# Optimization experiments

Measured on AMD Instinct MI355X. Metric: run time of the kernel, lower is better.

The kernel has to match this reference:

```python
import jax, jax.numpy as jnp
import numpy as np

B = 4          # clouds per batch
N_PER = 8192   # points per cloud
RATIO = 0.5
M = int(N_PER * RATIO)   # sampled centroids per cloud
R = 0.2        # radius
K = 64         # max_num_neighbors
C_IN = 64


def setup_inputs() -> dict:
    key = jax.random.key(0)
    k1, k2, k3, k4 = jax.random.split(key, 4)
    N = B * N_PER
    x = jax.random.normal(k1, (N, C_IN), dtype=jnp.float32)
    pos = jax.random.uniform(k2, (N, 3), dtype=jnp.float32)  # unit cube
    batch = jnp.repeat(jnp.arange(B, dtype=jnp.int32), N_PER)
    W1 = jax.random.normal(k3, (C_IN + 3, 64), dtype=jnp.float32) * (1.0 / np.sqrt(C_IN + 3))
    b1 = jnp.zeros((64,), dtype=jnp.float32)
    W2 = jax.random.normal(k4, (64, 128), dtype=jnp.float32) * (1.0 / np.sqrt(64))
    b2 = jnp.zeros((128,), dtype=jnp.float32)
    return {"x": x, "pos": pos, "batch": batch, "W1": W1, "b1": b1, "W2": W2, "b2": b2}


def _fps(posb):
    """Farthest point sampling, vectorized over clouds. posb: [B, n, 3] -> idx [B, M]."""
    d0 = jnp.sum((posb - posb[:, :1]) ** 2, axis=-1)  # dist^2 to seed point 0: [B, n]

    def step(dists, _):
        far = jnp.argmax(dists, axis=1)                              # [B]
        newp = jnp.take_along_axis(posb, far[:, None, None], axis=1)  # [B, 1, 3]
        d = jnp.sum((posb - newp) ** 2, axis=-1)                      # [B, n]
        return jnp.minimum(dists, d), far.astype(jnp.int32)

    _, rest = jax.lax.scan(step, d0, None, length=M - 1)  # rest: [M-1, B]
    return jnp.concatenate([jnp.zeros((B, 1), jnp.int32), rest.T], axis=1)  # [B, M]


def reference(x, pos, batch, W1, b1, W2, b2):
    posb = pos.reshape(B, N_PER, 3)
    xb = x.reshape(B, N_PER, C_IN)

    # --- fps ---
    idx = _fps(posb)                                         # [B, M]
    q = jnp.take_along_axis(posb, idx[:, :, None], axis=1)   # sampled centroids [B, M, 3]

    # --- radius query: K nearest neighbors within radius R (same cloud) ---
    d2 = jnp.sum((q[:, :, None, :] - posb[:, None, :, :]) ** 2, axis=-1)  # [B, M, n]
    neg = jnp.where(d2 <= R * R, -d2, -jnp.inf)
    vals, nbr = jax.lax.top_k(neg, K)                        # [B, M, K]
    valid = vals > -jnp.inf                                  # neighbor mask

    # --- PointNetConv: gather -> MLP -> masked max aggregation ---
    bidx = jnp.arange(B)[:, None, None]
    xj = xb[bidx, nbr]                                       # [B, M, K, C_IN]
    rel = posb[bidx, nbr] - q[:, :, None, :]                 # [B, M, K, 3]
    feat = jnp.concatenate([xj, rel], axis=-1)               # [B, M, K, C_IN+3]
    h = jax.nn.relu(feat @ W1 + b1)                          # [B, M, K, 64]
    h = jax.nn.relu(h @ W2 + b2)                             # [B, M, K, 128]
    h = jnp.where(valid[..., None], h, -jnp.inf)
    out = jnp.max(h, axis=2)                                 # [B, M, 128]; self-edge guarantees >=1 valid

    x_out = out.reshape(B * M, 128)
    pos_out = q.reshape(B * M, 3)
    batch_out = jnp.repeat(jnp.arange(B, dtype=batch.dtype), M)
    return x_out, pos_out, batch_out
```

## Files before the change

### kernel.cpp

```cpp
#include <hip/hip_runtime.h>
#include <stdint.h>

#define NPER 8192
#define NB 4
#define MPER 4096
#define MTOT (NB*MPER)
#define KNB 64
#define CIN 64
#define R2C 0.04f

#define POSOUT_OFF (MTOT*128)
#define BATCH_OFF  (MTOT*128 + MTOT*3)


#define FPS_T 1024
#define PTS 8
#define NCELL 512

#define OFF_XS 0
#define OFF_YS (OFF_XS + NPER*4)
#define OFF_ZS (OFF_YS + NPER*4)
#define OFF_OS (OFF_ZS + NPER*4)
#define OFF_WIN (OFF_OS + NPER*2)
#define OFF_HIST (OFF_WIN + MPER*2)
#define OFF_SCAN (OFF_HIST + NCELL*4)
#define OFF_SLOT (OFF_SCAN + NCELL*4)
#define OFF_SID0 (OFF_SLOT + 24)
#define FPS_LDS  (OFF_SID0 + 8)

__device__ inline unsigned morton3(unsigned ix, unsigned iy, unsigned iz) {
  unsigned m = 0;
#pragma unroll
  for (int b = 0; b < 3; ++b)
    m |= (((ix >> b) & 1u) << (3*b + 2)) | (((iy >> b) & 1u) << (3*b + 1)) |
         (((iz >> b) & 1u) << (3*b));
  return m;
}

template<int CTRL>
__device__ __forceinline__ unsigned dppmax(unsigned v) {
  unsigned t = (unsigned)__builtin_amdgcn_update_dpp(
      0, (int)v, CTRL, 0xf, 0xf, true);
  return v > t ? v : t;
}
__device__ __forceinline__ unsigned wave_max_u32(unsigned v) {
  v = dppmax<0x111>(v);
  v = dppmax<0x112>(v);
  v = dppmax<0x114>(v);
  v = dppmax<0x118>(v);
  v = dppmax<0x142>(v);
  v = dppmax<0x143>(v);
  return (unsigned)__builtin_amdgcn_readlane((int)v, 63);
}

__global__ __launch_bounds__(1024) void k_fps(const float* __restrict__ pos,
                                              float* __restrict__ dout)
{
  extern __shared__ char smem[];
  float* Xs = (float*)(smem + OFF_XS);
  float* Ys = (float*)(smem + OFF_YS);
  float* Zs = (float*)(smem + OFF_ZS);
  unsigned short* Os = (unsigned short*)(smem + OFF_OS);
  unsigned short* winb = (unsigned short*)(smem + OFF_WIN);
  unsigned* hist = (unsigned*)(smem + OFF_HIST);
  unsigned* scanb = (unsigned*)(smem + OFF_SCAN);
  unsigned long long* slot3 = (unsigned long long*)(smem + OFF_SLOT);
  unsigned* sid0p = (unsigned*)(smem + OFF_SID0);

  const int b = blockIdx.x;
  const int tid = threadIdx.x;
  const float* pb = pos + (size_t)b * NPER * 3;
  float* qo = dout + POSOUT_OFF + (size_t)b * MPER * 3;

  if (tid < NCELL) hist[tid] = 0u;
  if (tid == 0) { slot3[0] = 0ull; slot3[1] = 0ull; slot3[2] = 0ull; }
  __syncthreads();

  float sxv[PTS], syv[PTS], szv[PTS];
  unsigned cellv[PTS];
#pragma unroll
  for (int k = 0; k < PTS; ++k) {
    int i = k * FPS_T + tid;
    sxv[k] = pb[i*3+0]; syv[k] = pb[i*3+1]; szv[k] = pb[i*3+2];
    unsigned ix = min(7u, (unsigned)(int)(sxv[k] * 8.0f));
    unsigned iy = min(7u, (unsigned)(int)(syv[k] * 8.0f));
    unsigned iz = min(7u, (unsigned)(int)(szv[k] * 8.0f));
    cellv[k] = morton3(ix, iy, iz);
    atomicAdd(&hist[cellv[k]], 1u);
  }
  __syncthreads();
  if (tid < NCELL) scanb[tid] = hist[tid];
  __syncthreads();
  for (int s = 1; s < NCELL; s <<= 1) {
    unsigned v = 0u;
    if (tid >= s && tid < NCELL) v = scanb[tid - s];
    __syncthreads();
    if (tid >= s && tid < NCELL) scanb[tid] += v;
    __syncthreads();
  }
  if (tid < NCELL) hist[tid] = scanb[tid] - hist[tid];
  __syncthreads();
#pragma unroll
  for (int k = 0; k < PTS; ++k) {
    unsigned dst = atomicAdd(&hist[cellv[k]], 1u);
    int orig = k * FPS_T + tid;
    Xs[dst] = sxv[k]; Ys[dst] = syv[k]; Zs[dst] = szv[k];
    Os[dst] = (unsigned short)orig;
    if (orig == 0) *sid0p = dst;
  }
  __syncthreads();
  float X[PTS], Y[PTS], Z[PTS], D[PTS];
  unsigned RK[PTS];
  float bxlo = 3.402823466e+38f, bylo = bxlo, bzlo = bxlo;
  float bxhi = -bxlo, byhi = bxhi, bzhi = bxhi;
#pragma unroll
  for (int k = 0; k < PTS; ++k) {
    int s = tid * PTS + k;
    X[k] = Xs[s]; Y[k] = Ys[s]; Z[k] = Zs[s];
    unsigned orig = Os[s];
    RK[k] = ((unsigned)(NPER - 1 - orig) << 13) | (unsigned)s;
    D[k] = 3.402823466e+38f;
    bxlo = fminf(bxlo, X[k]); bxhi = fmaxf(bxhi, X[k]);
    bylo = fminf(bylo, Y[k]); byhi = fmaxf(byhi, Y[k]);
    bzlo = fminf(bzlo, Z[k]); bzhi = fmaxf(bzhi, Z[k]);
  }

  unsigned long long tkey = 0ull, wkey = 0ull;
  float lmax = 3.402823466e+38f;
  unsigned sidx = *sid0p;
  for (int m = 1; m < MPER; ++m) {
    const float cx = Xs[sidx], cy = Ys[sidx], cz = Zs[sidx];
    if (tid == 0) winb[m-1] = (unsigned short)sidx;
    if (tid == 1) slot3[(m+1) % 3] = 0ull;
    float ax = fmaxf(fmaxf(__fsub_rn(bxlo, cx), __fsub_rn(cx, bxhi)), 0.0f);
    float ay = fmaxf(fmaxf(__fsub_rn(bylo, cy), __fsub_rn(cy, byhi)), 0.0f);
    float az = fmaxf(fmaxf(__fsub_rn(bzlo, cz), __fsub_rn(cz, bzhi)), 0.0f);
    float lb = ax*ax + ay*ay + az*az;
    bool upd = (lb * 0.99988f) < lmax;
    if (__ballot(upd) != 0ull) {
      if (upd) {
        unsigned long long bk = 0ull;
#pragma unroll
        for (int k = 0; k < PTS; ++k) {
          float dx = __fsub_rn(X[k], cx);
          float dy = __fsub_rn(Y[k], cy);
          float dz = __fsub_rn(Z[k], cz);
          float s = __fadd_rn(__fadd_rn(__fmul_rn(dx,dx), __fmul_rn(dy,dy)),
                              __fmul_rn(dz,dz));
          float dn = fminf(D[k], s);
          D[k] = dn;
          unsigned long long kk =
            ((unsigned long long)__float_as_uint(dn) << 26) | RK[k];
          bk = (kk > bk) ? kk : bk;
        }
        tkey = bk;
        lmax = __uint_as_float((unsigned)(bk >> 26));
      }
      unsigned hi = (unsigned)(tkey >> 26);
      unsigned M = wave_max_u32(hi);
      unsigned rk = (unsigned)tkey & 0x3FFFFFFu;
      unsigned cand = (hi == M) ? (~rk & 0x3FFFFFFu) : 0u;
      unsigned C = wave_max_u32(cand);
      wkey = ((unsigned long long)M << 26) | (~C & 0x3FFFFFFu);
    }
    if ((tid & 63) == 0) atomicMax(&slot3[m % 3], wkey);
    __syncthreads();
    sidx = (unsigned)(slot3[m % 3] & 0x1FFFull);
  }
  if (tid == 0) winb[MPER-1] = (unsigned short)sidx;
  __syncthreads();
  for (int e = tid; e < MPER; e += FPS_T) {
    unsigned s = winb[e];
    qo[e*3+0] = Xs[s]; qo[e*3+1] = Ys[s]; qo[e*3+2] = Zs[s];
  }
}

#define SCAP 512
__global__ __launch_bounds__(256) void k_radius(const float* __restrict__ pos,
    float* __restrict__ dout, unsigned short* __restrict__ nbr,
    int* __restrict__ cnt)
{
  __shared__ unsigned candH[4][SCAP];
  __shared__ unsigned candL[4][SCAP];
  const int wid = threadIdx.x >> 6, lane = threadIdx.x & 63;
  const int m = blockIdx.x * 4 + wid;
  const int b = m >> 12;
  const float* pb = pos + (size_t)b * NPER * 3;
  const float* q = dout + POSOUT_OFF + (size_t)m * 3;
  const float qx = q[0], qy = q[1], qz = q[2];
  unsigned cw = 0;
  for (int it = 0; it < NPER/64; ++it) {
    int i = (it << 6) + lane;
    float dx = __fsub_rn(qx, pb[i*3+0]);
    float dy = __fsub_rn(qy, pb[i*3+1]);
    float dz = __fsub_rn(qz, pb[i*3+2]);
    float d2 = __fadd_rn(__fadd_rn(__fmul_rn(dx,dx), __fmul_rn(dy,dy)),
                         __fmul_rn(dz,dz));
    bool in = (d2 <= R2C);
    unsigned long long mk = __ballot(in);
    unsigned pre = (unsigned)__popcll(mk & ((1ull << lane) - 1ull));
    if (in) {
      unsigned slot = cw + pre;
      if (slot < SCAP) {
        candH[wid][slot] = __float_as_uint(d2);
        candL[wid][slot] = (unsigned)i;
      }
    }
    cw += (unsigned)__popcll(mk);
  }
  if (cw > SCAP) cw = SCAP;
  for (int s = (int)cw + lane; s < SCAP; s += 64) {
    candH[wid][s] = 0xFFFFFFFFu; candL[wid][s] = 0xFFFFFFFFu;
  }
  __syncthreads();
  for (int k = 2; k <= SCAP; k <<= 1) {
    for (int j = k >> 1; j > 0; j >>= 1) {
#pragma unroll
      for (int s = 0; s < SCAP/128; ++s) {
        int t = lane + (s << 6);
        int e = ((t & ~(j-1)) << 1) | (t & (j-1));
        int p = e | j;
        unsigned aH = candH[wid][e], aL = candL[wid][e];
        unsigned cH = candH[wid][p], cL = candL[wid][p];
        bool agt = (aH > cH) || (aH == cH && aL > cL);
        bool asc = ((e & k) == 0);
        bool sw = asc ? agt : !agt && (aH != cH || aL != cL);
        if (sw) {
          candH[wid][e] = cH; candL[wid][e] = cL;
          candH[wid][p] = aH; candL[wid][p] = aL;
        }
      }
      __syncthreads();
    }
  }
  int kk = (int)cw; if (kk > KNB) kk = KNB;
  nbr[(size_t)m*KNB + lane] =
    (lane < kk) ? (unsigned short)(candL[wid][lane] & 0xFFFFu)
                : (unsigned short)0;
  if (lane == 0) {
    cnt[m] = kk;
    dout[BATCH_OFF + m] = (float)b;
  }
}

__global__ __launch_bounds__(128) void k_conv(
    const float* __restrict__ x, const float* __restrict__ pos,
    const float* __restrict__ W1, const float* __restrict__ b1,
    const float* __restrict__ W2, const float* __restrict__ b2,
    const unsigned short* __restrict__ nbr, const int* __restrict__ cntp,
    float* __restrict__ dout)
{
  __shared__ __align__(16) float bufA[68*68];
  __shared__ __align__(16) float bufB[68*68];
  __shared__ unsigned short nbr_s[64];
  __shared__ float qv[3];
  __shared__ int cnt_s;
  const int t = threadIdx.x;
  const int m = blockIdx.x;
  const int b = m >> 12;
  if (t < 64) nbr_s[t] = nbr[(size_t)m*KNB + t];
  else if (t == 64) cnt_s = cntp[m];
  else if (t >= 65 && t < 68) qv[t-65] = dout[POSOUT_OFF + (size_t)m*3 + (t-65)];
  for (int e = t; e < 67*64; e += 128) {
    int ch = e >> 6, h = e & 63;
    bufB[ch*68 + h] = W1[e];
  }
  __syncthreads();
  {
    const int ch = t & 63, jj = t >> 6;
    const size_t xb = (size_t)b * NPER * CIN;
    for (int j0 = 0; j0 < 64; j0 += 2) {
      int j = j0 + jj;
      int r = nbr_s[j];
      bufA[ch*68 + j] = x[xb + (size_t)r*CIN + ch];
    }
  }
  {
    const size_t pbb = (size_t)b * NPER * 3;
    for (int e = t; e < 192; e += 128) {
      int j = e & 63, d = e >> 6;
      int r = nbr_s[j];
      bufA[(64+d)*68 + j] = pos[pbb + (size_t)r*3 + d] - qv[d];
    }
  }
  __syncthreads();

  const int jg = t & 7, hg = t >> 3;
  const int j0 = jg << 3;
  const int h0 = hg << 2;
  float acc[4][8];
#pragma unroll
  for (int hh = 0; hh < 4; ++hh)
#pragma unroll
    for (int j = 0; j < 8; ++j) acc[hh][j] = 0.0f;
  for (int ch = 0; ch < 67; ++ch) {
    const float4 fa = *(const float4*)&bufA[ch*68 + j0];
    const float4 fb = *(const float4*)&bufA[ch*68 + j0 + 4];
    const float4 w  = *(const float4*)&bufB[ch*68 + h0];
    const float ws4[4] = {w.x, w.y, w.z, w.w};
    const float fj[8] = {fa.x, fa.y, fa.z, fa.w, fb.x, fb.y, fb.z, fb.w};
#pragma unroll
    for (int hh = 0; hh < 4; ++hh)
#pragma unroll
      for (int j = 0; j < 8; ++j)
        acc[hh][j] += ws4[hh] * fj[j];
  }
  __syncthreads();
  {
    const float4 bb = *(const float4*)&b1[h0];
    const float bv[4] = {bb.x, bb.y, bb.z, bb.w};
#pragma unroll
    for (int hh = 0; hh < 4; ++hh) {
      float4 o0, o1;
      o0.x = fmaxf(acc[hh][0] + bv[hh], 0.0f);
      o0.y = fmaxf(acc[hh][1] + bv[hh], 0.0f);
      o0.z = fmaxf(acc[hh][2] + bv[hh], 0.0f);
      o0.w = fmaxf(acc[hh][3] + bv[hh], 0.0f);
      o1.x = fmaxf(acc[hh][4] + bv[hh], 0.0f);
      o1.y = fmaxf(acc[hh][5] + bv[hh], 0.0f);
      o1.z = fmaxf(acc[hh][6] + bv[hh], 0.0f);
      o1.w = fmaxf(acc[hh][7] + bv[hh], 0.0f);
      *(float4*)&bufA[(h0+hh)*68 + j0] = o0;
      *(float4*)&bufA[(h0+hh)*68 + j0 + 4] = o1;
    }
  }
  const int c0 = hg << 3;
  float acc2[8][8];
#pragma unroll
  for (int c = 0; c < 8; ++c)
#pragma unroll
    for (int j = 0; j < 8; ++j) acc2[c][j] = 0.0f;
  for (int hc = 0; hc < 64; hc += 16) {
    __syncthreads();
    for (int e = t; e < 16*128; e += 128) {
      int hh = e >> 7, c = e & 127;
      bufB[hh*136 + c] = W2[(size_t)(hc+hh)*128 + c];
    }
    __syncthreads();
#pragma unroll
    for (int h = 0; h < 16; ++h) {
      const float4 ja = *(const float4*)&bufA[(hc+h)*68 + j0];
      const float4 jb = *(const float4*)&bufA[(hc+h)*68 + j0 + 4];
      const float4 wa = *(const float4*)&bufB[h*136 + c0];
      const float4 wb = *(const float4*)&bufB[h*136 + c0 + 4];
      const float hv[8] = {ja.x, ja.y, ja.z, ja.w, jb.x, jb.y, jb.z, jb.w};
      const float wv[8] = {wa.x, wa.y, wa.z, wa.w, wb.x, wb.y, wb.z, wb.w};
#pragma unroll
      for (int c = 0; c < 8; ++c)
#pragma unroll
        for (int j = 0; j < 8; ++j)
          acc2[c][j] += wv[c] * hv[j];
    }
  }
  const int cntv = cnt_s;
  const float4 b2a = *(const float4*)&b2[c0];
  const float4 b2b = *(const float4*)&b2[c0 + 4];
  const float bv2[8] = {b2a.x, b2a.y, b2a.z, b2a.w, b2b.x, b2b.y, b2b.z, b2b.w};
  float best[8];
#pragma unroll
  for (int c = 0; c < 8; ++c) {
    float v = -3.402823466e+38f;
#pragma unroll
    for (int j = 0; j < 8; ++j) {
      float hv = fmaxf(acc2[c][j] + bv2[c], 0.0f);
      v = (j0 + j < cntv) ? fmaxf(v, hv) : v;
    }
    best[c] = v;
  }
#pragma unroll
  for (int off = 1; off < 8; off <<= 1)
#pragma unroll
    for (int c = 0; c < 8; ++c)
      best[c] = fmaxf(best[c], __shfl_xor(best[c], off));
  if (jg == 0) {
    float4 o0 = {best[0], best[1], best[2], best[3]};
    float4 o1 = {best[4], best[5], best[6], best[7]};
    *(float4*)&dout[(size_t)m*128 + c0] = o0;
    *(float4*)&dout[(size_t)m*128 + c0 + 4] = o1;
  }
}

extern "C" void kernel_launch(void* const* d_in, const int* in_sizes, int n_in,
                              void* d_out, int out_size, void* d_ws, size_t ws_size,
                              hipStream_t stream) {
  const float* x   = (const float*)d_in[0];
  const float* pos = (const float*)d_in[1];
  const float* W1  = (const float*)d_in[3];
  const float* b1  = (const float*)d_in[4];
  const float* W2  = (const float*)d_in[5];
  const float* b2  = (const float*)d_in[6];
  float* dout = (float*)d_out;
  unsigned short* nbr = (unsigned short*)d_ws;
  int* cnt = (int*)((char*)d_ws + (size_t)MTOT*KNB*2);

  hipLaunchKernelGGL(k_fps,    dim3(NB),     dim3(FPS_T), FPS_LDS, stream, pos, dout);
  hipLaunchKernelGGL(k_radius, dim3(MTOT/4), dim3(256),   0, stream, pos, dout, nbr, cnt);
  hipLaunchKernelGGL(k_conv,   dim3(MTOT),   dim3(128),   0, stream,
                     x, pos, W1, b1, W2, b2, nbr, cnt, dout);
}
```

Measured before the change: 3.488 ms.

## Use cell-sorted point grid for radius query and pack FPS distance math

Result: faster. 3.354 ms (-3.8%).

```diff
diff --git a/kernel.cpp b/kernel.cpp
--- a/kernel.cpp
+++ b/kernel.cpp
@@ -12,6 +12,9 @@
 #define POSOUT_OFF (MTOT*128)
 #define BATCH_OFF  (MTOT*128 + MTOT*3)
 
+#define SSTR 30720
+
+typedef float v2f __attribute__((ext_vector_type(2)));
 
 #define FPS_T 1024
 #define PTS 8
@@ -28,15 +31,6 @@
 #define OFF_SID0 (OFF_SLOT + 24)
 #define FPS_LDS  (OFF_SID0 + 8)
 
-__device__ inline unsigned morton3(unsigned ix, unsigned iy, unsigned iz) {
-  unsigned m = 0;
-#pragma unroll
-  for (int b = 0; b < 3; ++b)
-    m |= (((ix >> b) & 1u) << (3*b + 2)) | (((iy >> b) & 1u) << (3*b + 1)) |
-         (((iz >> b) & 1u) << (3*b));
-  return m;
-}
-
 template<int CTRL>
 __device__ __forceinline__ unsigned dppmax(unsigned v) {
   unsigned t = (unsigned)__builtin_amdgcn_update_dpp(
@@ -56,6 +50,7 @@
 __global__ __launch_bounds__(1024) void k_fps(const float* __restrict__ pos,
                                               float* __restrict__ dout)
 {
+#pragma clang fp contract(off)
   extern __shared__ char smem[];
   float* Xs = (float*)(smem + OFF_XS);
   float* Ys = (float*)(smem + OFF_YS);
@@ -71,6 +66,10 @@
   const int tid = threadIdx.x;
   const float* pb = pos + (size_t)b * NPER * 3;
   float* qo = dout + POSOUT_OFF + (size_t)b * MPER * 3;
+  float* scrb = dout + (size_t)b * SSTR;
+  float* gSX = scrb; float* gSY = scrb + 8192; float* gSZ = scrb + 16384;
+  unsigned* gSO = (unsigned*)(scrb + 24576);
+  unsigned* gCS = (unsigned*)(scrb + 28672);
 
   if (tid < NCELL) hist[tid] = 0u;
   if (tid == 0) { slot3[0] = 0ull; slot3[1] = 0ull; slot3[2] = 0ull; }
@@ -85,7 +84,7 @@
     unsigned ix = min(7u, (unsigned)(int)(sxv[k] * 8.0f));
     unsigned iy = min(7u, (unsigned)(int)(syv[k] * 8.0f));
     unsigned iz = min(7u, (unsigned)(int)(szv[k] * 8.0f));
-    cellv[k] = morton3(ix, iy, iz);
+    cellv[k] = (ix << 6) | (iy << 3) | iz;
     atomicAdd(&hist[cellv[k]], 1u);
   }
   __syncthreads();
@@ -98,7 +97,11 @@
     if (tid >= s && tid < NCELL) scanb[tid] += v;
     __syncthreads();
   }
-  if (tid < NCELL) hist[tid] = scanb[tid] - hist[tid];
+  if (tid < NCELL) {
+    hist[tid] = scanb[tid] - hist[tid];
+    gCS[tid+1] = scanb[tid];
+  }
+  if (tid == 0) gCS[0] = 0u;
   __syncthreads();
 #pragma unroll
   for (int k = 0; k < PTS; ++k) {
@@ -109,20 +112,26 @@
     if (orig == 0) *sid0p = dst;
   }
   __syncthreads();
-  float X[PTS], Y[PTS], Z[PTS], D[PTS];
+  for (int e = tid; e < NPER; e += FPS_T) {
+    gSX[e] = Xs[e]; gSY[e] = Ys[e]; gSZ[e] = Zs[e];
+  }
+  for (int e = tid; e < NPER/2; e += FPS_T)
+    gSO[e] = ((const unsigned*)Os)[e];
+  v2f Xp[4], Yp[4], Zp[4], Dp[4];
   unsigned RK[PTS];
   float bxlo = 3.402823466e+38f, bylo = bxlo, bzlo = bxlo;
   float bxhi = -bxlo, byhi = bxhi, bzhi = bxhi;
 #pragma unroll
   for (int k = 0; k < PTS; ++k) {
     int s = tid * PTS + k;
-    X[k] = Xs[s]; Y[k] = Ys[s]; Z[k] = Zs[s];
+    float xx = Xs[s], yy = Ys[s], zz = Zs[s];
+    Xp[k>>1][k&1] = xx; Yp[k>>1][k&1] = yy; Zp[k>>1][k&1] = zz;
+    Dp[k>>1][k&1] = 3.402823466e+38f;
     unsigned orig = Os[s];
     RK[k] = ((unsigned)(NPER - 1 - orig) << 13) | (unsigned)s;
-    D[k] = 3.402823466e+38f;
-    bxlo = fminf(bxlo, X[k]); bxhi = fmaxf(bxhi, X[k]);
-    bylo = fminf(bylo, Y[k]); byhi = fmaxf(byhi, Y[k]);
-    bzlo = fminf(bzlo, Z[k]); bzhi = fmaxf(bzhi, Z[k]);
+    bxlo = fminf(bxlo, xx); bxhi = fmaxf(bxhi, xx);
+    bylo = fminf(bylo, yy); byhi = fmaxf(byhi, yy);
+    bzlo = fminf(bzlo, zz); bzhi = fmaxf(bzhi, zz);
   }
 
   unsigned long long tkey = 0ull, wkey = 0ull;
@@ -139,29 +148,42 @@
     bool upd = (lb * 0.99988f) < lmax;
     if (__ballot(upd) != 0ull) {
       if (upd) {
-        unsigned long long bk = 0ull;
-#pragma unroll
-        for (int k = 0; k < PTS; ++k) {
-          float dx = __fsub_rn(X[k], cx);
-          float dy = __fsub_rn(Y[k], cy);
-          float dz = __fsub_rn(Z[k], cz);
-          float s = __fadd_rn(__fadd_rn(__fmul_rn(dx,dx), __fmul_rn(dy,dy)),
-                              __fmul_rn(dz,dz));
-          float dn = fminf(D[k], s);
-          D[k] = dn;
-          unsigned long long kk =
-            ((unsigned long long)__float_as_uint(dn) << 26) | RK[k];
-          bk = (kk > bk) ? kk : bk;
+        v2f cx2 = {cx, cx}, cy2 = {cy, cy}, cz2 = {cz, cz};
+        v2f dnp[4];
+        float bd = -1.0f;
+#pragma unroll
+        for (int p = 0; p < 4; ++p) {
+          v2f dx = Xp[p] - cx2;
+          v2f dy = Yp[p] - cy2;
+          v2f dz = Zp[p] - cz2;
+          v2f s = (dx*dx + dy*dy) + dz*dz;
+          v2f dn;
+          dn.x = fminf(Dp[p].x, s.x);
+          dn.y = fminf(Dp[p].y, s.y);
+          Dp[p] = dn; dnp[p] = dn;
+          bd = fmaxf(bd, fmaxf(dn.x, dn.y));
         }
-        tkey = bk;
-        lmax = __uint_as_float((unsigned)(bk >> 26));
+        unsigned brk = 0u;
+#pragma unroll
+        for (int p = 0; p < 4; ++p) {
+          brk = (dnp[p].x == bd) ? max(brk, RK[2*p])   : brk;
+          brk = (dnp[p].y == bd) ? max(brk, RK[2*p+1]) : brk;
+        }
+        tkey = ((unsigned long long)__float_as_uint(bd) << 26) | brk;
+        lmax = bd;
       }
       unsigned hi = (unsigned)(tkey >> 26);
       unsigned M = wave_max_u32(hi);
       unsigned rk = (unsigned)tkey & 0x3FFFFFFu;
-      unsigned cand = (hi == M) ? (~rk & 0x3FFFFFFu) : 0u;
-      unsigned C = wave_max_u32(cand);
-      wkey = ((unsigned long long)M << 26) | (~C & 0x3FFFFFFu);
+      unsigned long long msk = __ballot(hi == M);
+      unsigned lo;
+      if (__popcll(msk) == 1) {
+        int ln = (int)__builtin_ctzll(msk);
+        lo = (unsigned)__builtin_amdgcn_readlane((int)rk, ln);
+      } else {
+        lo = wave_max_u32((hi == M) ? rk : 0u);
+      }
+      wkey = ((unsigned long long)M << 26) | lo;
     }
     if ((tid & 63) == 0) atomicMax(&slot3[m % 3], wkey);
     __syncthreads();
@@ -185,28 +207,51 @@
   const int wid = threadIdx.x >> 6, lane = threadIdx.x & 63;
   const int m = blockIdx.x * 4 + wid;
   const int b = m >> 12;
-  const float* pb = pos + (size_t)b * NPER * 3;
+  const float* scrb = dout + (size_t)b * SSTR;
+  const float* SX = scrb;
+  const float* SY = scrb + 8192;
+  const float* SZ = scrb + 16384;
+  const unsigned short* SO = (const unsigned short*)(scrb + 24576);
+  const unsigned* CS = (const unsigned*)(scrb + 28672);
   const float* q = dout + POSOUT_OFF + (size_t)m * 3;
   const float qx = q[0], qy = q[1], qz = q[2];
+  const int ixc = min(7, (int)(qx * 8.0f));
+  const int iyc = min(7, (int)(qy * 8.0f));
+  const int izc = min(7, (int)(qz * 8.0f));
+  const int izlo = max(izc-2, 0), izhi = min(izc+2, 7);
+  unsigned s0v = 0u, s1v = 0u;
+  {
+    int ix = ixc + lane / 5 - 2;
+    int iy = iyc + lane % 5 - 2;
+    if (lane < 25 && ix >= 0 && ix < 8 && iy >= 0 && iy < 8) {
+      int cb = (ix << 6) | (iy << 3);
+      s0v = CS[cb + izlo];
+      s1v = CS[cb + izhi + 1];
+    }
+  }
   unsigned cw = 0;
-  for (int it = 0; it < NPER/64; ++it) {
-    int i = (it << 6) + lane;
-    float dx = __fsub_rn(qx, pb[i*3+0]);
-    float dy = __fsub_rn(qy, pb[i*3+1]);
-    float dz = __fsub_rn(qz, pb[i*3+2]);
-    float d2 = __fadd_rn(__fadd_rn(__fmul_rn(dx,dx), __fmul_rn(dy,dy)),
-                         __fmul_rn(dz,dz));
-    bool in = (d2 <= R2C);
-    unsigned long long mk = __ballot(in);
-    unsigned pre = (unsigned)__popcll(mk & ((1ull << lane) - 1ull));
-    if (in) {
-      unsigned slot = cw + pre;
-      if (slot < SCAP) {
-        candH[wid][slot] = __float_as_uint(d2);
-        candL[wid][slot] = (unsigned)i;
+  for (int seg = 0; seg < 25; ++seg) {
+    unsigned s0 = (unsigned)__builtin_amdgcn_readlane((int)s0v, seg);
+    unsigned s1 = (unsigned)__builtin_amdgcn_readlane((int)s1v, seg);
+    for (unsigned i0 = s0; i0 < s1; i0 += 64) {
+      unsigned i = i0 + (unsigned)lane;
+      float dx = __fsub_rn(qx, SX[i]);
+      float dy = __fsub_rn(qy, SY[i]);
+      float dz = __fsub_rn(qz, SZ[i]);
+      float d2 = __fadd_rn(__fadd_rn(__fmul_rn(dx,dx), __fmul_rn(dy,dy)),
+                           __fmul_rn(dz,dz));
+      bool in = (i < s1) && (d2 <= R2C);
+      unsigned long long mk = __ballot(in);
+      unsigned pre = (unsigned)__popcll(mk & ((1ull << lane) - 1ull));
+      if (in) {
+        unsigned slot = cw + pre;
+        if (slot < SCAP) {
+          candH[wid][slot] = __float_as_uint(d2);
+          candL[wid][slot] = (unsigned)SO[i];
+        }
       }
-    }
-    cw += (unsigned)__popcll(mk);
+      cw += (unsigned)__popcll(mk);
+    }
   }
   if (cw > SCAP) cw = SCAP;
   for (int s = (int)cw + lane; s < SCAP; s += 64) {
```
